# Performance work log

Hardware: AMD Instinct MI355X
Metric: run time of the kernel (lower is better)

Reference implementation:

```python
import jax, jax.numpy as jnp
import numpy as np

H = 12          # num_attention_heads
D = 64          # num_embed_hidden == attention_head_size
B, T = 4, 2048
SCALE = 1.0 / np.sqrt(D)


def setup_inputs() -> dict:
    key = jax.random.key(0)
    ks = jax.random.split(key, 7)
    P = H * D  # num_attn_proj = 768
    s = 1.0 / np.sqrt(D)
    return {
        "hidden_states": jax.random.normal(ks[0], (B, T, D), dtype=jnp.float32),
        "attention_mask": jnp.ones((B, T), dtype=jnp.float32),
        "Wq": jax.random.normal(ks[1], (D, P), dtype=jnp.float32) * s,
        "bq": jnp.zeros((P,), dtype=jnp.float32),
        "Wk": jax.random.normal(ks[2], (D, P), dtype=jnp.float32) * s,
        "bk": jnp.zeros((P,), dtype=jnp.float32),
        "Wv": jax.random.normal(ks[3], (D, P), dtype=jnp.float32) * s,
        "bv": jnp.zeros((P,), dtype=jnp.float32),
    }


def reference(hidden_states, attention_mask, Wq, bq, Wk, bk, Wv, bv):
    b, t, _ = hidden_states.shape
    # QKV projections -> [B, H, T, D]
    def proj(W, bias):
        return (hidden_states @ W + bias).reshape(b, t, H, D).transpose(0, 2, 1, 3)
    q = proj(Wq, bq)
    k = proj(Wk, bk)
    v = proj(Wv, bv)
    # [B, H, T, T] scores
    scores = jnp.einsum("bhqd,bhkd->bhqk", q, k) * SCALE
    mask = (1.0 - attention_mask)[:, None, None, :] * -10000.0
    scores = scores + mask
    attn = jax.nn.softmax(scores, axis=-1)
    # dropout is identity in eval mode
    y = jnp.einsum("bhqk,bhkd->bhqd", attn, v)
    return y.transpose(0, 2, 1, 3).reshape(b, t, H * D)
```

## Files before the change

### kernel.cpp

```cpp
#include <hip/hip_runtime.h>
#include <hip/hip_bf16.h>

#define NH 12
#define HD 64
#define NB 4
#define SEQ 2048
#define NP 768
#define LOG2E 1.44269504f
#define MASK_L2 14426.9504f

typedef __bf16 bf16x8 __attribute__((ext_vector_type(8)));
typedef __bf16 bf16x2 __attribute__((ext_vector_type(2)));
typedef float f32x2 __attribute__((ext_vector_type(2)));
typedef float f32x4 __attribute__((ext_vector_type(4)));
typedef float f32x16 __attribute__((ext_vector_type(16)));
typedef unsigned u32x4 __attribute__((ext_vector_type(4)));

static __device__ __forceinline__ bf16x8 load_bf16x8(const __bf16* p) {
    return *reinterpret_cast<const bf16x8*>(p);
}
static __device__ __forceinline__ float hw_exp2(float x) {
    return __builtin_amdgcn_exp2f(x);
}
static __device__ __forceinline__ unsigned cvtpk2(float lo, float hi) {
    f32x2 t; t[0] = lo; t[1] = hi;
    return __builtin_bit_cast(unsigned, __builtin_convertvector(t, bf16x2));
}

__global__ __launch_bounds__(256) void qkv_kernel(
    const float* __restrict__ hidden,
    const float* __restrict__ Wq, const float* __restrict__ Wk,
    const float* __restrict__ Wv,
    const float* __restrict__ bq, const float* __restrict__ bk,
    const float* __restrict__ bv,
    __bf16* __restrict__ Qw, __bf16* __restrict__ Kf, __bf16* __restrict__ Vf)
{
    __shared__ __bf16 wtileT[64][72];
    __shared__ __bf16 ot[64][72];

    const int tid  = threadIdx.x;
    const int lane = tid & 63;
    const int w    = tid >> 6;
    const int g    = lane >> 4;
    const int n    = lane & 15;
    const int n32  = lane & 31;
    const int hi   = lane >> 5;

    const int row0 = blockIdx.x * 64;
    const int gi   = blockIdx.y;
    const int b_   = row0 >> 11;
    const int t0   = row0 & (SEQ - 1);
    const int kb64 = t0 >> 6;

    const float* hrow = hidden + (size_t)(row0 + w * 16 + n) * HD + 8 * g;
    f32x4 h0 = *(const f32x4*)(hrow);
    f32x4 h1 = *(const f32x4*)(hrow + 4);
    f32x4 h2 = *(const f32x4*)(hrow + 32);
    f32x4 h3 = *(const f32x4*)(hrow + 36);
    bf16x8 a0, a1;
    #pragma unroll
    for (int j = 0; j < 4; ++j) {
        a0[j]     = (__bf16)h0[j];
        a0[j + 4] = (__bf16)h1[j];
        a1[j]     = (__bf16)h2[j];
        a1[j + 4] = (__bf16)h3[j];
    }

    const int dr   = tid >> 2;
    const int coff = (tid & 3) * 16;

    for (int tt = 0; tt < 18; ++tt) {
        const int tile_id = gi * 18 + tt;
        const int proj    = tile_id / 12;
        const int head    = tile_id % 12;
        const int bh      = b_ * NH + head;
        const float* W    = proj == 0 ? Wq : (proj == 1 ? Wk : Wv);
        const float* bias = proj == 0 ? bq : (proj == 1 ? bk : bv);
        const float qs    = (proj == 0) ? 0.125f * LOG2E : 1.0f;

        const float* wr = W + (size_t)dr * NP + head * 64 + coff;
        f32x4 x0 = *(const f32x4*)(wr);
        f32x4 x1 = *(const f32x4*)(wr + 4);
        f32x4 x2 = *(const f32x4*)(wr + 8);
        f32x4 x3 = *(const f32x4*)(wr + 12);
        #pragma unroll
        for (int i = 0; i < 4; ++i) {
            wtileT[coff + i     ][dr] = (__bf16)(x0[i] * qs);
            wtileT[coff + 4 + i ][dr] = (__bf16)(x1[i] * qs);
            wtileT[coff + 8 + i ][dr] = (__bf16)(x2[i] * qs);
            wtileT[coff + 12 + i][dr] = (__bf16)(x3[i] * qs);
        }
        __syncthreads();

        #pragma unroll
        for (int dt = 0; dt < 4; ++dt) {
            const bf16x8 b0 = *(const bf16x8*)&wtileT[dt * 16 + n][8 * g];
            const bf16x8 b1 = *(const bf16x8*)&wtileT[dt * 16 + n][32 + 8 * g];
            f32x4 acc = {0.f, 0.f, 0.f, 0.f};
            acc = __builtin_amdgcn_mfma_f32_16x16x32_bf16(a0, b0, acc, 0, 0, 0);
            acc = __builtin_amdgcn_mfma_f32_16x16x32_bf16(a1, b1, acc, 0, 0, 0);
            const float bb = bias[head * 64 + dt * 16 + n] * qs;
            #pragma unroll
            for (int r = 0; r < 4; ++r)
                ot[w * 16 + 4 * g + r][dt * 16 + n] = (__bf16)(acc[r] + bb);
        }
        __syncthreads();

        if (proj == 0) {
            __bf16* dst = Qw + ((size_t)bh * SEQ + t0 + w * 16) * HD;
            const int tr = lane >> 2;
            const int d0 = (lane & 3) * 16;
            *(bf16x8*)(dst + (size_t)tr * HD + d0)     = *(const bf16x8*)&ot[w * 16 + tr][d0];
            *(bf16x8*)(dst + (size_t)tr * HD + d0 + 8) = *(const bf16x8*)&ot[w * 16 + tr][d0 + 8];
        } else if (proj == 1) {
            __bf16* base = Kf + (size_t)bh * SEQ * HD + (size_t)kb64 * 4096;
            #pragma unroll
            for (int sub = 0; sub < 2; ++sub) {
                const bf16x8 fr = *(const bf16x8*)&ot[sub * 32 + n32][w * 16 + 8 * hi];
                *(bf16x8*)(base + (size_t)(w * 2 + sub) * 512 + lane * 8) = fr;
            }
        } else {
            __bf16* base = Vf + (size_t)bh * SEQ * HD + (size_t)kb64 * 4096;
            #pragma unroll
            for (int dsub = 0; dsub < 2; ++dsub) {
                bf16x8 v;
                #pragma unroll
                for (int j = 0; j < 8; ++j)
                    v[j] = ot[w * 16 + ((j & 3) + 8 * (j >> 2) + 4 * hi)][dsub * 32 + n32];
                *(bf16x8*)(base + (size_t)(w * 2 + dsub) * 512 + lane * 8) = v;
            }
        }
    }
}

__global__ __launch_bounds__(256, 4) void flash_attn_kernel(
    const __bf16* __restrict__ Qw, const __bf16* __restrict__ Kf,
    const __bf16* __restrict__ Vf, const float* __restrict__ amask,
    float* __restrict__ out)
{
    __shared__ __align__(16) char smem[35328];
    __bf16* mdd = (__bf16*)smem;
    float (*et)[32][68] = (float(*)[32][68])smem;
    float* lrow = (float*)(smem + 34816);

    const int tid  = threadIdx.x;
    const int lane = tid & 63;
    const int w    = tid >> 6;
    const int n32  = lane & 31;
    const int hi   = lane >> 5;

    const int bid    = blockIdx.x;
    const int xcd    = bid & 7;
    const int slot   = bid >> 3;
    const int bh     = xcd * 6 + (slot >> 6);
    const int qchunk = slot & 63;
    const int b_     = bh / NH;
    const int h      = bh % NH;
    const int q0     = qchunk * 32;

    const float* mp = amask + (size_t)b_ * SEQ;
    #pragma unroll
    for (int i = 0; i < 8; ++i) {
        const int idx = w * 512 + i * 64 + lane;
        mdd[idx] = (__bf16)fmaf(mp[idx], MASK_L2, -MASK_L2);
    }

    const __bf16* Qrow = Qw + ((size_t)bh * SEQ + q0 + n32) * HD + 8 * hi;
    bf16x8 qf[4];
    #pragma unroll
    for (int d = 0; d < 4; ++d) qf[d] = load_bf16x8(Qrow + d * 16);

    bf16x8 qone;
    #pragma unroll
    for (int j = 0; j < 8; ++j) qone[j] = (__bf16)0.0f;
    if (hi == 0) qone[0] = (__bf16)1.0f;

    const __bf16* kfb_ = Kf + (size_t)bh * SEQ * HD + (size_t)lane * 8;
    const __bf16* vfb_ = Vf + (size_t)bh * SEQ * HD + (size_t)lane * 8;

    f32x16 o0 = {0,0,0,0,0,0,0,0,0,0,0,0,0,0,0,0};
    f32x16 o1 = {0,0,0,0,0,0,0,0,0,0,0,0,0,0,0,0};
    f32x2 lsl2 = {0.f, 0.f};

    const int kstart = w * 512;
    for (int it = 0; it < 8; ++it) {
        const int kb = kstart + it * 64;
        const size_t foff = (size_t)(kb >> 6) * 4096;

        bf16x8 kfa[4], kfb[4], vf0[4], vf1[4];
        #pragma unroll
        for (int d = 0; d < 4; ++d) {
            kfa[d] = load_bf16x8(kfb_ + foff + (size_t)(2 * d) * 512);
            kfb[d] = load_bf16x8(kfb_ + foff + (size_t)(2 * d + 1) * 512);
        }
        #pragma unroll
        for (int c = 0; c < 4; ++c) {
            vf0[c] = load_bf16x8(vfb_ + foff + (size_t)(2 * c) * 512);
            vf1[c] = load_bf16x8(vfb_ + foff + (size_t)(2 * c + 1) * 512);
        }

        bf16x8 maa, mab;
        #pragma unroll
        for (int j = 0; j < 8; ++j) { maa[j] = (__bf16)0.0f; mab[j] = (__bf16)0.0f; }
        maa[0] = mdd[kb + n32];
        mab[0] = mdd[kb + 32 + n32];

        f32x16 sa = {0,0,0,0,0,0,0,0,0,0,0,0,0,0,0,0};
        #pragma unroll
        for (int d = 0; d < 4; ++d)
            sa = __builtin_amdgcn_mfma_f32_32x32x16_bf16(kfa[d], qf[d], sa, 0, 0, 0);
        sa = __builtin_amdgcn_mfma_f32_32x32x16_bf16(maa, qone, sa, 0, 0, 0);

        bf16x8 P0, P1;
        {
            float p[16];
            #pragma unroll
            for (int r = 0; r < 16; ++r) p[r] = hw_exp2(sa[r]);
            u32x4 B0, B1;
            #pragma unroll
            for (int i = 0; i < 4; ++i) {
                B0[i] = cvtpk2(p[2 * i],     p[2 * i + 1]);
                B1[i] = cvtpk2(p[8 + 2 * i], p[8 + 2 * i + 1]);
            }
            #pragma unroll
            for (int i = 0; i < 8; ++i) {
                f32x2 t; t[0] = p[2 * i]; t[1] = p[2 * i + 1];
                lsl2 += t;
            }
            P0 = __builtin_bit_cast(bf16x8, B0);
            P1 = __builtin_bit_cast(bf16x8, B1);
        }
        o0 = __builtin_amdgcn_mfma_f32_32x32x16_bf16(vf0[0], P0, o0, 0, 0, 0);
        o1 = __builtin_amdgcn_mfma_f32_32x32x16_bf16(vf1[0], P0, o1, 0, 0, 0);
        o0 = __builtin_amdgcn_mfma_f32_32x32x16_bf16(vf0[1], P1, o0, 0, 0, 0);
        o1 = __builtin_amdgcn_mfma_f32_32x32x16_bf16(vf1[1], P1, o1, 0, 0, 0);

        f32x16 sb = {0,0,0,0,0,0,0,0,0,0,0,0,0,0,0,0};
        #pragma unroll
        for (int d = 0; d < 4; ++d)
            sb = __builtin_amdgcn_mfma_f32_32x32x16_bf16(kfb[d], qf[d], sb, 0, 0, 0);
        sb = __builtin_amdgcn_mfma_f32_32x32x16_bf16(mab, qone, sb, 0, 0, 0);

        bf16x8 P2, P3;
        {
            float p[16];
            #pragma unroll
            for (int r = 0; r < 16; ++r) p[r] = hw_exp2(sb[r]);
            u32x4 B0, B1;
            #pragma unroll
            for (int i = 0; i < 4; ++i) {
                B0[i] = cvtpk2(p[2 * i],     p[2 * i + 1]);
                B1[i] = cvtpk2(p[8 + 2 * i], p[8 + 2 * i + 1]);
            }
            #pragma unroll
            for (int i = 0; i < 8; ++i) {
                f32x2 t; t[0] = p[2 * i]; t[1] = p[2 * i + 1];
                lsl2 += t;
            }
            P2 = __builtin_bit_cast(bf16x8, B0);
            P3 = __builtin_bit_cast(bf16x8, B1);
        }
        o0 = __builtin_amdgcn_mfma_f32_32x32x16_bf16(vf0[2], P2, o0, 0, 0, 0);
        o1 = __builtin_amdgcn_mfma_f32_32x32x16_bf16(vf1[2], P2, o1, 0, 0, 0);
        o0 = __builtin_amdgcn_mfma_f32_32x32x16_bf16(vf0[3], P3, o0, 0, 0, 0);
        o1 = __builtin_amdgcn_mfma_f32_32x32x16_bf16(vf1[3], P3, o1, 0, 0, 0);
    }

    float rs = lsl2[0] + lsl2[1];
    rs += __shfl_xor(rs, 32);

    __syncthreads();

    #pragma unroll
    for (int r = 0; r < 16; ++r) {
        const int dl = (r & 3) + 8 * (r >> 2) + 4 * hi;
        et[w][n32][dl]      = o0[r];
        et[w][n32][32 + dl] = o1[r];
    }
    if (lane < 32) lrow[w * 32 + n32] = rs;
    __syncthreads();

    const int q  = tid >> 3;
    const int d0 = (tid & 7) * 8;
    const float linv = 1.0f / (lrow[q] + lrow[32 + q] + lrow[64 + q] + lrow[96 + q]);
    f32x4 acc0 = {0,0,0,0}, acc1 = {0,0,0,0};
    #pragma unroll
    for (int ww = 0; ww < 4; ++ww) {
        acc0 += *(const f32x4*)&et[ww][q][d0];
        acc1 += *(const f32x4*)&et[ww][q][d0 + 4];
    }
    float* orow = out + ((size_t)(b_ * SEQ + q0 + q)) * NP + h * HD + d0;
    f32x4 r0, r1;
    #pragma unroll
    for (int i = 0; i < 4; ++i) { r0[i] = acc0[i] * linv; r1[i] = acc1[i] * linv; }
    *(f32x4*)(orow)     = r0;
    *(f32x4*)(orow + 4) = r1;
}

extern "C" void kernel_launch(void* const* d_in, const int* in_sizes, int n_in,
                              void* d_out, int out_size, void* d_ws, size_t ws_size,
                              hipStream_t stream) {
    const float* hidden = (const float*)d_in[0];
    const float* amask  = (const float*)d_in[1];
    const float* Wq     = (const float*)d_in[2];
    const float* bq     = (const float*)d_in[3];
    const float* Wk     = (const float*)d_in[4];
    const float* bk     = (const float*)d_in[5];
    const float* Wv     = (const float*)d_in[6];
    const float* bv     = (const float*)d_in[7];
    float* out = (float*)d_out;

    const size_t elems = (size_t)NB * NH * SEQ * HD;
    __bf16* Qw = (__bf16*)d_ws;
    __bf16* Kf = Qw + elems;
    __bf16* Vf = Kf + elems;

    qkv_kernel<<<dim3(128, 2), 256, 0, stream>>>(
        hidden, Wq, Wk, Wv, bq, bk, bv, Qw, Kf, Vf);

    flash_attn_kernel<<<dim3(3072), 256, 0, stream>>>(
        Qw, Kf, Vf, amask, out);
}
```

Measured before the change: 177.7 us.

## Pretranspose QKV weights to bf16 in a separate kernel and widen the projection grid

A new small kernel transposes and scales the Q/K/V weights into a bf16 [3*768][64] workspace buffer. The projection kernel then reads MFMA B-fragments straight from global memory instead of staging each weight tile through LDS with barriers. Each block now handles 6 tiles instead of 18, so the grid grows from 256 to 768 blocks. Barriers are kept only around the K path, which reads across waves. The cost is an extra kernel launch, extra workspace, and uncached global fragment loads.

```diff
diff --git a/kernel.cpp b/kernel.cpp
--- a/kernel.cpp
+++ b/kernel.cpp
@@ -27,15 +27,36 @@
     return __builtin_bit_cast(unsigned, __builtin_convertvector(t, bf16x2));
 }
 
+__global__ __launch_bounds__(256) void wt_kernel(
+    const float* __restrict__ Wq, const float* __restrict__ Wk,
+    const float* __restrict__ Wv, __bf16* __restrict__ Wt)
+{
+    __shared__ float tile[64][69];
+    const int by = blockIdx.y;
+    const float* W = by == 0 ? Wq : (by == 1 ? Wk : Wv);
+    const float scale = (by == 0) ? 0.125f * LOG2E : 1.0f;
+    const int p0 = blockIdx.x * 64;
+    const int tl = threadIdx.x & 63;
+    const int tq = threadIdx.x >> 6;
+    #pragma unroll
+    for (int i = 0; i < 16; ++i) {
+        const int d = tq + 4 * i;
+        tile[tl][d] = W[(size_t)d * NP + p0 + tl];
+    }
+    __syncthreads();
+    #pragma unroll
+    for (int i = 0; i < 16; ++i) {
+        const int pl = tq + 4 * i;
+        Wt[((size_t)by * NP + p0 + pl) * HD + tl] = (__bf16)(tile[pl][tl] * scale);
+    }
+}
+
 __global__ __launch_bounds__(256) void qkv_kernel(
-    const float* __restrict__ hidden,
-    const float* __restrict__ Wq, const float* __restrict__ Wk,
-    const float* __restrict__ Wv,
+    const float* __restrict__ hidden, const __bf16* __restrict__ Wt,
     const float* __restrict__ bq, const float* __restrict__ bk,
     const float* __restrict__ bv,
     __bf16* __restrict__ Qw, __bf16* __restrict__ Kf, __bf16* __restrict__ Vf)
 {
-    __shared__ __bf16 wtileT[64][72];
     __shared__ __bf16 ot[64][72];
 
     const int tid  = threadIdx.x;
@@ -66,36 +87,20 @@
         a1[j + 4] = (__bf16)h3[j];
     }
 
-    const int dr   = tid >> 2;
-    const int coff = (tid & 3) * 16;
-
-    for (int tt = 0; tt < 18; ++tt) {
-        const int tile_id = gi * 18 + tt;
+    for (int tt = 0; tt < 6; ++tt) {
+        const int tile_id = gi * 6 + tt;
         const int proj    = tile_id / 12;
         const int head    = tile_id % 12;
         const int bh      = b_ * NH + head;
-        const float* W    = proj == 0 ? Wq : (proj == 1 ? Wk : Wv);
         const float* bias = proj == 0 ? bq : (proj == 1 ? bk : bv);
         const float qs    = (proj == 0) ? 0.125f * LOG2E : 1.0f;
 
-        const float* wr = W + (size_t)dr * NP + head * 64 + coff;
-        f32x4 x0 = *(const f32x4*)(wr);
-        f32x4 x1 = *(const f32x4*)(wr + 4);
-        f32x4 x2 = *(const f32x4*)(wr + 8);
-        f32x4 x3 = *(const f32x4*)(wr + 12);
-        #pragma unroll
-        for (int i = 0; i < 4; ++i) {
-            wtileT[coff + i     ][dr] = (__bf16)(x0[i] * qs);
-            wtileT[coff + 4 + i ][dr] = (__bf16)(x1[i] * qs);
-            wtileT[coff + 8 + i ][dr] = (__bf16)(x2[i] * qs);
-            wtileT[coff + 12 + i][dr] = (__bf16)(x3[i] * qs);
-        }
-        __syncthreads();
-
         #pragma unroll
         for (int dt = 0; dt < 4; ++dt) {
-            const bf16x8 b0 = *(const bf16x8*)&wtileT[dt * 16 + n][8 * g];
-            const bf16x8 b1 = *(const bf16x8*)&wtileT[dt * 16 + n][32 + 8 * g];
+            const __bf16* wp = Wt +
+                ((size_t)proj * NP + head * 64 + dt * 16 + n) * HD + 8 * g;
+            const bf16x8 b0 = load_bf16x8(wp);
+            const bf16x8 b1 = load_bf16x8(wp + 32);
             f32x4 acc = {0.f, 0.f, 0.f, 0.f};
             acc = __builtin_amdgcn_mfma_f32_16x16x32_bf16(a0, b0, acc, 0, 0, 0);
             acc = __builtin_amdgcn_mfma_f32_16x16x32_bf16(a1, b1, acc, 0, 0, 0);
@@ -104,7 +109,6 @@
             for (int r = 0; r < 4; ++r)
                 ot[w * 16 + 4 * g + r][dt * 16 + n] = (__bf16)(acc[r] + bb);
         }
-        __syncthreads();
 
         if (proj == 0) {
             __bf16* dst = Qw + ((size_t)bh * SEQ + t0 + w * 16) * HD;
@@ -113,12 +117,14 @@
             *(bf16x8*)(dst + (size_t)tr * HD + d0)     = *(const bf16x8*)&ot[w * 16 + tr][d0];
             *(bf16x8*)(dst + (size_t)tr * HD + d0 + 8) = *(const bf16x8*)&ot[w * 16 + tr][d0 + 8];
         } else if (proj == 1) {
+            __syncthreads();
             __bf16* base = Kf + (size_t)bh * SEQ * HD + (size_t)kb64 * 4096;
             #pragma unroll
             for (int sub = 0; sub < 2; ++sub) {
                 const bf16x8 fr = *(const bf16x8*)&ot[sub * 32 + n32][w * 16 + 8 * hi];
                 *(bf16x8*)(base + (size_t)(w * 2 + sub) * 512 + lane * 8) = fr;
             }
+            __syncthreads();
         } else {
             __bf16* base = Vf + (size_t)bh * SEQ * HD + (size_t)kb64 * 4096;
             #pragma unroll
@@ -314,9 +320,12 @@
     __bf16* Qw = (__bf16*)d_ws;
     __bf16* Kf = Qw + elems;
     __bf16* Vf = Kf + elems;
-
-    qkv_kernel<<<dim3(128, 2), 256, 0, stream>>>(
-        hidden, Wq, Wk, Wv, bq, bk, bv, Qw, Kf, Vf);
+    __bf16* Wt = Vf + elems;
+
+    wt_kernel<<<dim3(12, 3), 256, 0, stream>>>(Wq, Wk, Wv, Wt);
+
+    qkv_kernel<<<dim3(128, 6), 256, 0, stream>>>(
+        hidden, Wt, bq, bk, bv, Qw, Kf, Vf);
 
     flash_attn_kernel<<<dim3(3072), 256, 0, stream>>>(
         Qw, Kf, Vf, amask, out);
```

Measured after the change: 174.1 us. 1.02x faster.

## Software-pipeline QK^T one half-tile ahead of softmax and PV

Applied to the files above, without the earlier changes.

Restructures the inner attention loop into 16 half-tile steps. The scores for the next 32-key chunk are computed while the current chunk's exp and PV MFMAs run, and K fragments are prefetched two steps ahead, so the matrix units can overlap with the exp/convert work and load latency is hidden. Launch bounds drop from 4 to 3 waves-per-EU to give the extra live registers room, at the cost of lower occupancy. The final iterations wrap around and prefetch redundant K blocks.

```diff
diff --git a/kernel.cpp b/kernel.cpp
--- a/kernel.cpp
+++ b/kernel.cpp
@@ -133,7 +133,7 @@
     }
 }
 
-__global__ __launch_bounds__(256, 4) void flash_attn_kernel(
+__global__ __launch_bounds__(256, 3) void flash_attn_kernel(
     const __bf16* __restrict__ Qw, const __bf16* __restrict__ Kf,
     const __bf16* __restrict__ Vf, const float* __restrict__ amask,
     float* __restrict__ out)
@@ -183,87 +183,89 @@
     f32x2 lsl2 = {0.f, 0.f};
 
     const int kstart = w * 512;
-    for (int it = 0; it < 8; ++it) {
-        const int kb = kstart + it * 64;
-        const size_t foff = (size_t)(kb >> 6) * 4096;
-
-        bf16x8 kfa[4], kfb[4], vf0[4], vf1[4];
+    const int blk0   = kstart >> 6;
+
+    bf16x8 kcur[4], knxt[4];
+    {
+        const size_t f0 = (size_t)blk0 * 4096;
         #pragma unroll
         for (int d = 0; d < 4; ++d) {
-            kfa[d] = load_bf16x8(kfb_ + foff + (size_t)(2 * d) * 512);
-            kfb[d] = load_bf16x8(kfb_ + foff + (size_t)(2 * d + 1) * 512);
-        }
-        #pragma unroll
-        for (int c = 0; c < 4; ++c) {
-            vf0[c] = load_bf16x8(vfb_ + foff + (size_t)(2 * c) * 512);
-            vf1[c] = load_bf16x8(vfb_ + foff + (size_t)(2 * c + 1) * 512);
-        }
-
-        bf16x8 maa, mab;
-        #pragma unroll
-        for (int j = 0; j < 8; ++j) { maa[j] = (__bf16)0.0f; mab[j] = (__bf16)0.0f; }
-        maa[0] = mdd[kb + n32];
-        mab[0] = mdd[kb + 32 + n32];
-
-        f32x16 sa = {0,0,0,0,0,0,0,0,0,0,0,0,0,0,0,0};
+            kcur[d] = load_bf16x8(kfb_ + f0 + (size_t)(2 * d) * 512);
+            knxt[d] = load_bf16x8(kfb_ + f0 + (size_t)(2 * d + 1) * 512);
+        }
+    }
+
+    f32x16 scur = {0,0,0,0,0,0,0,0,0,0,0,0,0,0,0,0};
+    {
+        bf16x8 mf;
+        #pragma unroll
+        for (int j = 0; j < 8; ++j) mf[j] = (__bf16)0.0f;
+        mf[0] = mdd[kstart + n32];
         #pragma unroll
         for (int d = 0; d < 4; ++d)
-            sa = __builtin_amdgcn_mfma_f32_32x32x16_bf16(kfa[d], qf[d], sa, 0, 0, 0);
-        sa = __builtin_amdgcn_mfma_f32_32x32x16_bf16(maa, qone, sa, 0, 0, 0);
+            scur = __builtin_amdgcn_mfma_f32_32x32x16_bf16(kcur[d], qf[d], scur, 0, 0, 0);
+        scur = __builtin_amdgcn_mfma_f32_32x32x16_bf16(mf, qone, scur, 0, 0, 0);
+    }
+
+    for (int hh = 0; hh < 16; ++hh) {
+        const int h2 = (hh + 2) & 15;
+        const int h1 = (hh + 1) & 15;
+        const int p  = hh & 1;
+        const int p2 = h2 & 1;
+        const size_t foff_h  = (size_t)(blk0 + (hh >> 1)) * 4096;
+        const size_t foff_h2 = (size_t)(blk0 + (h2 >> 1)) * 4096;
+
+        bf16x8 kpre[4];
+        #pragma unroll
+        for (int d = 0; d < 4; ++d)
+            kpre[d] = load_bf16x8(kfb_ + foff_h2 + (size_t)(2 * d + p2) * 512);
+
+        bf16x8 v0[2], v1[2];
+        #pragma unroll
+        for (int e = 0; e < 2; ++e) {
+            const int c = 2 * p + e;
+            v0[e] = load_bf16x8(vfb_ + foff_h + (size_t)(2 * c) * 512);
+            v1[e] = load_bf16x8(vfb_ + foff_h + (size_t)(2 * c + 1) * 512);
+        }
+
+        bf16x8 mf1;
+        #pragma unroll
+        for (int j = 0; j < 8; ++j) mf1[j] = (__bf16)0.0f;
+        mf1[0] = mdd[kstart + h1 * 32 + n32];
+        f32x16 snxt = {0,0,0,0,0,0,0,0,0,0,0,0,0,0,0,0};
+        #pragma unroll
+        for (int d = 0; d < 4; ++d)
+            snxt = __builtin_amdgcn_mfma_f32_32x32x16_bf16(knxt[d], qf[d], snxt, 0, 0, 0);
+        snxt = __builtin_amdgcn_mfma_f32_32x32x16_bf16(mf1, qone, snxt, 0, 0, 0);
 
         bf16x8 P0, P1;
         {
-            float p[16];
-            #pragma unroll
-            for (int r = 0; r < 16; ++r) p[r] = hw_exp2(sa[r]);
+            float pp[16];
+            #pragma unroll
+            for (int r = 0; r < 16; ++r) pp[r] = hw_exp2(scur[r]);
             u32x4 B0, B1;
             #pragma unroll
             for (int i = 0; i < 4; ++i) {
-                B0[i] = cvtpk2(p[2 * i],     p[2 * i + 1]);
-                B1[i] = cvtpk2(p[8 + 2 * i], p[8 + 2 * i + 1]);
+                B0[i] = cvtpk2(pp[2 * i],     pp[2 * i + 1]);
+                B1[i] = cvtpk2(pp[8 + 2 * i], pp[8 + 2 * i + 1]);
             }
             #pragma unroll
             for (int i = 0; i < 8; ++i) {
-                f32x2 t; t[0] = p[2 * i]; t[1] = p[2 * i + 1];
+                f32x2 t; t[0] = pp[2 * i]; t[1] = pp[2 * i + 1];
                 lsl2 += t;
             }
             P0 = __builtin_bit_cast(bf16x8, B0);
             P1 = __builtin_bit_cast(bf16x8, B1);
         }
-        o0 = __builtin_amdgcn_mfma_f32_32x32x16_bf16(vf0[0], P0, o0, 0, 0, 0);
-        o1 = __builtin_amdgcn_mfma_f32_32x32x16_bf16(vf1[0], P0, o1, 0, 0, 0);
-        o0 = __builtin_amdgcn_mfma_f32_32x32x16_bf16(vf0[1], P1, o0, 0, 0, 0);
-        o1 = __builtin_amdgcn_mfma_f32_32x32x16_bf16(vf1[1], P1, o1, 0, 0, 0);
-
-        f32x16 sb = {0,0,0,0,0,0,0,0,0,0,0,0,0,0,0,0};
-        #pragma unroll
-        for (int d = 0; d < 4; ++d)
-            sb = __builtin_amdgcn_mfma_f32_32x32x16_bf16(kfb[d], qf[d], sb, 0, 0, 0);
-        sb = __builtin_amdgcn_mfma_f32_32x32x16_bf16(mab, qone, sb, 0, 0, 0);
-
-        bf16x8 P2, P3;
-        {
-            float p[16];
-            #pragma unroll
-            for (int r = 0; r < 16; ++r) p[r] = hw_exp2(sb[r]);
-            u32x4 B0, B1;
-            #pragma unroll
-            for (int i = 0; i < 4; ++i) {
-                B0[i] = cvtpk2(p[2 * i],     p[2 * i + 1]);
-                B1[i] = cvtpk2(p[8 + 2 * i], p[8 + 2 * i + 1]);
-            }
-            #pragma unroll
-            for (int i = 0; i < 8; ++i) {
-                f32x2 t; t[0] = p[2 * i]; t[1] = p[2 * i + 1];
-                lsl2 += t;
-            }
-            P2 = __builtin_bit_cast(bf16x8, B0);
-            P3 = __builtin_bit_cast(bf16x8, B1);
-        }
-        o0 = __builtin_amdgcn_mfma_f32_32x32x16_bf16(vf0[2], P2, o0, 0, 0, 0);
-        o1 = __builtin_amdgcn_mfma_f32_32x32x16_bf16(vf1[2], P2, o1, 0, 0, 0);
-        o0 = __builtin_amdgcn_mfma_f32_32x32x16_bf16(vf0[3], P3, o0, 0, 0, 0);
-        o1 = __builtin_amdgcn_mfma_f32_32x32x16_bf16(vf1[3], P3, o1, 0, 0, 0);
+
+        o0 = __builtin_amdgcn_mfma_f32_32x32x16_bf16(v0[0], P0, o0, 0, 0, 0);
+        o1 = __builtin_amdgcn_mfma_f32_32x32x16_bf16(v1[0], P0, o1, 0, 0, 0);
+        o0 = __builtin_amdgcn_mfma_f32_32x32x16_bf16(v0[1], P1, o0, 0, 0, 0);
+        o1 = __builtin_amdgcn_mfma_f32_32x32x16_bf16(v1[1], P1, o1, 0, 0, 0);
+
+        scur = snxt;
+        #pragma unroll
+        for (int d = 0; d < 4; ++d) knxt[d] = kpre[d];
     }
 
     float rs = lsl2[0] + lsl2[1];
```

Result: slower. 182.5 us (+2.7%).
